# Kernel tuning notes

Measured on AMD Instinct MI355X. Metric: run time of the kernel, lower is better.

The kernel has to match this reference:

```python
import jax, jax.numpy as jnp
import numpy as np

N = 20000        # nodes
E = 320000       # edges (before self-loops)
V = 5000         # vocab size for each of the 5 categorical fields
L = 20           # padded token list length per node
SF = 16          # scalar feature count
ED = 32          # embedding_dim
HC = 128         # hidden_channels
NH = 4           # num_heads (conv1)
B = 8            # graphs in batch
DIN = SF + 5 * ED  # 176


def setup_inputs() -> dict:
    key = jax.random.key(0)
    ks = jax.random.split(key, 24)
    inp = {
        "x_scalar": jax.random.normal(ks[0], (N, SF), jnp.float32),
        "x_opcode": jax.random.randint(ks[1], (N, L), 0, V),
        "x_source": jax.random.randint(ks[2], (N, L), 0, V),
        "x_sink": jax.random.randint(ks[3], (N, L), 0, V),
        "x_string_manip": jax.random.randint(ks[4], (N, L), 0, V),
        "x_payload": jax.random.randint(ks[5], (N, L), 0, V),
        "edge_index": jax.random.randint(ks[6], (2, E), 0, N),
        "batch": jnp.sort(jax.random.randint(ks[7], (N,), 0, B)),
        # embedding tables (padding row 0 contributes nothing via the mask)
        "emb_opcode": jax.random.normal(ks[8], (V, ED), jnp.float32),
        "emb_source": jax.random.normal(ks[9], (V, ED), jnp.float32),
        "emb_sink": jax.random.normal(ks[10], (V, ED), jnp.float32),
        "emb_string_manip": jax.random.normal(ks[11], (V, ED), jnp.float32),
        "emb_payload": jax.random.normal(ks[12], (V, ED), jnp.float32),
        # LayerNorm params
        "ln_g": jnp.ones((DIN,), jnp.float32),
        "ln_b": jnp.zeros((DIN,), jnp.float32),
        # GATConv 1: in=DIN, out=HC, heads=NH
        "W1": jax.random.normal(ks[13], (DIN, NH * HC), jnp.float32) / np.sqrt(DIN),
        "a_src1": jax.random.normal(ks[14], (NH, HC), jnp.float32) / np.sqrt(HC),
        "a_dst1": jax.random.normal(ks[15], (NH, HC), jnp.float32) / np.sqrt(HC),
        "b1": jnp.zeros((NH * HC,), jnp.float32),
        # GATConv 2: in=NH*HC, out=HC, heads=1
        "W2": jax.random.normal(ks[16], (NH * HC, HC), jnp.float32) / np.sqrt(NH * HC),
        "a_src2": jax.random.normal(ks[17], (1, HC), jnp.float32) / np.sqrt(HC),
        "a_dst2": jax.random.normal(ks[18], (1, HC), jnp.float32) / np.sqrt(HC),
        "b2": jnp.zeros((HC,), jnp.float32),
    }
    return inp


def _masked_mean(table, idx):
    # embeds * (idx != 0) summed over token dim, divided by token count
    emb = table[idx]                                   # [N, L, ED]
    mask = (idx != 0).astype(table.dtype)[..., None]   # [N, L, 1]
    return (emb * mask).sum(1) / (mask.sum(1) + 1e-9)


def _layer_norm(x, g, b, eps=1e-5):
    mu = x.mean(-1, keepdims=True)
    var = ((x - mu) ** 2).mean(-1, keepdims=True)
    return (x - mu) * jax.lax.rsqrt(var + eps) * g + b


def _gat(x, src, dst, W, a_src, a_dst, bias, n):
    # PyG GATConv (eval mode: attention dropout off), self-loops already in src/dst
    h_, c = a_src.shape
    h = (x @ W).reshape(n, h_, c)                      # [N, H, C]
    al_s = (h * a_src).sum(-1)                         # [N, H]
    al_d = (h * a_dst).sum(-1)                         # [N, H]
    e = jax.nn.leaky_relu(al_s[src] + al_d[dst], 0.2)  # [E, H]
    m = jax.ops.segment_max(e, dst, num_segments=n)    # per-dst max for stability
    ex = jnp.exp(e - m[dst])
    den = jax.ops.segment_sum(ex, dst, num_segments=n)
    alpha = ex / (den[dst] + 1e-16)                    # per-dst softmax
    msg = h[src] * alpha[:, :, None]                   # [E, H, C]
    out = jax.ops.segment_sum(msg, dst, num_segments=n)
    return out.reshape(n, h_ * c) + bias


def reference(x_scalar, x_opcode, x_source, x_sink, x_string_manip, x_payload,
              edge_index, batch,
              emb_opcode, emb_source, emb_sink, emb_string_manip, emb_payload,
              ln_g, ln_b, W1, a_src1, a_dst1, b1, W2, a_src2, a_dst2, b2):
    n = x_scalar.shape[0]
    feats = jnp.concatenate([
        x_scalar,
        _masked_mean(emb_opcode, x_opcode),
        _masked_mean(emb_source, x_source),
        _masked_mean(emb_sink, x_sink),
        _masked_mean(emb_string_manip, x_string_manip),
        _masked_mean(emb_payload, x_payload),
    ], axis=1)                                         # [N, DIN]
    # GATConv adds self-loops by default
    loops = jnp.arange(n, dtype=edge_index.dtype)
    src = jnp.concatenate([edge_index[0], loops])
    dst = jnp.concatenate([edge_index[1], loops])
    x = jax.nn.elu(_gat(_layer_norm(feats, ln_g, ln_b), src, dst, W1, a_src1, a_dst1, b1, n))
    x = jax.nn.elu(_gat(x, src, dst, W2, a_src2, a_dst2, b2, n))
    return jax.ops.segment_max(x, batch, num_segments=B)  # global_max_pool -> [B, HC]
```

## Files before the change

kernel.cpp:

```cpp
#include <hip/hip_runtime.h>
#include <math.h>

#define SF 16
#define ED 32
#define LTOK 20
#define DIN 176
#define KP1 192
#define HC 128

typedef _Float16 f16x8 __attribute__((ext_vector_type(8)));
typedef float f32x4 __attribute__((ext_vector_type(4)));

static __device__ __forceinline__ float leaky02(float x) { return x >= 0.f ? x : 0.2f * x; }
static __device__ __forceinline__ float eluf(float x)    { return x > 0.f ? x : expm1f(x); }
static __device__ __forceinline__ unsigned short f2h(float f)
{
  _Float16 h = (_Float16)f;
  return __builtin_bit_cast(unsigned short, h);
}
static __device__ __forceinline__ float h2f(unsigned short u)
{
  return (float)__builtin_bit_cast(_Float16, u);
}
static __device__ __forceinline__ float readlane_f(float v, int j)
{
  return __int_as_float(__builtin_amdgcn_readlane(__float_as_int(v), j));
}

__global__ __launch_bounds__(256)
void prep_combined_kernel(const float* __restrict__ W1, const float* __restrict__ W2,
                          unsigned short* __restrict__ W1t, unsigned short* __restrict__ W2t,
                          const float* __restrict__ as1, const float* __restrict__ ad1,
                          float* __restrict__ vs, float* __restrict__ vd,
                          int* __restrict__ deg, unsigned* __restrict__ pool,
                          int N, int poolN)
{
  const int nb1 = (512 * KP1 + 255) / 256;
  const int nb2 = (HC * 512 + 255) / 256;
  const int nb3 = (N + 255) / 256;
  const int nb4 = (poolN + 255) / 256;
  int bid = blockIdx.x;
  if (bid < nb1) {
    int i = bid * 256 + threadIdx.x;
    if (i < 512 * KP1) {
      int n = i / KP1, k = i - n * KP1;
      W1t[i] = f2h((k < DIN) ? W1[(size_t)k * 512 + n] : 0.f);
    }
    return;
  }
  bid -= nb1;
  if (bid < nb2) {
    int i = bid * 256 + threadIdx.x;
    if (i < HC * 512) {
      int n = i / 512, k = i - n * 512;
      W2t[i] = f2h(W2[(size_t)k * HC + n]);
    }
    return;
  }
  bid -= nb2;
  if (bid < nb3) {
    int i = bid * 256 + threadIdx.x;
    if (i < N) deg[i] = 0;
    return;
  }
  bid -= nb3;
  if (bid < nb4) {
    int i = bid * 256 + threadIdx.x;
    if (i < poolN) pool[i] = 0x00800000u;
    return;
  }
  bid -= nb4;
  {
    int k = bid;
    int h = threadIdx.x >> 6, lane = threadIdx.x & 63;
    const float* row = W1 + (size_t)k * 512 + h * HC;
    float s = row[lane] * as1[h * HC + lane] + row[lane + 64] * as1[h * HC + lane + 64];
    float d = row[lane] * ad1[h * HC + lane] + row[lane + 64] * ad1[h * HC + lane + 64];
    #pragma unroll
    for (int off = 32; off; off >>= 1) { s += __shfl_down(s, off); d += __shfl_down(d, off); }
    if (lane == 0) { vs[k * 4 + h] = s; vd[k * 4 + h] = d; }
  }
}

__global__ __launch_bounds__(256)
void feat_ln_kernel(const float* __restrict__ xs,
                    const int* __restrict__ i0, const int* __restrict__ i1,
                    const int* __restrict__ i2, const int* __restrict__ i3,
                    const int* __restrict__ i4,
                    const float* __restrict__ e0, const float* __restrict__ e1,
                    const float* __restrict__ e2, const float* __restrict__ e3,
                    const float* __restrict__ e4,
                    const float* __restrict__ g, const float* __restrict__ b,
                    const float4* __restrict__ vs, const float4* __restrict__ vd,
                    unsigned short* __restrict__ out,
                    float* __restrict__ als, float* __restrict__ ald, int N)
{
  __shared__ int toks[4][5 * LTOK];
  int w = threadIdx.x >> 6, l = threadIdx.x & 63;
  int n = blockIdx.x * 4 + w;
  if (n >= N) return;

  for (int q = l; q < 5 * LTOK; q += 64) {
    int f = q / LTOK, j = q - f * LTOK;
    const int* ip = (f == 0) ? i0 : (f == 1) ? i1 : (f == 2) ? i2 : (f == 3) ? i3 : i4;
    toks[w][q] = ip[n * LTOK + j];
  }

  float v[3];
  #pragma unroll
  for (int r = 0; r < 3; ++r) {
    int c = l + r * 64;
    float val = 0.f;
    if (c < SF) {
      val = xs[n * SF + c];
    } else if (c < DIN) {
      int f  = (c - SF) >> 5;
      int ch = (c - SF) & 31;
      const float* ep = (f == 0) ? e0 : (f == 1) ? e1 : (f == 2) ? e2 : (f == 3) ? e3 : e4;
      float vals[LTOK];
      #pragma unroll
      for (int j = 0; j < LTOK; ++j)
        vals[j] = ep[toks[w][f * LTOK + j] * ED + ch];
      float sum = 0.f, cnt = 0.f;
      #pragma unroll
      for (int j = 0; j < LTOK; ++j)
        if (toks[w][f * LTOK + j] != 0) { sum += vals[j]; cnt += 1.f; }
      val = sum / (cnt + 1e-9f);
    }
    v[r] = val;
  }

  float p  = v[0] + v[1] + v[2];
  float p2 = v[0] * v[0] + v[1] * v[1] + v[2] * v[2];
  #pragma unroll
  for (int off = 32; off; off >>= 1) { p += __shfl_xor(p, off); p2 += __shfl_xor(p2, off); }
  float mu   = p * (1.f / DIN);
  float var  = fmaxf(p2 * (1.f / DIN) - mu * mu, 0.f);
  float rstd = rsqrtf(var + 1e-5f);

  float pr[8] = {0.f, 0.f, 0.f, 0.f, 0.f, 0.f, 0.f, 0.f};
  #pragma unroll
  for (int r = 0; r < 3; ++r) {
    int c = l + r * 64;
    float y = 0.f;
    if (c < DIN) {
      y = (v[r] - mu) * rstd * g[c] + b[c];
      float4 s4 = vs[c], d4 = vd[c];
      pr[0] += y * s4.x; pr[1] += y * s4.y; pr[2] += y * s4.z; pr[3] += y * s4.w;
      pr[4] += y * d4.x; pr[5] += y * d4.y; pr[6] += y * d4.z; pr[7] += y * d4.w;
    }
    if (c < KP1) out[(size_t)n * KP1 + c] = f2h(y);
  }
  #pragma unroll
  for (int j = 0; j < 8; ++j)
    #pragma unroll
    for (int off = 32; off; off >>= 1) pr[j] += __shfl_xor(pr[j], off);
  if (l == 0) {
    als[n * 4 + 0] = pr[0]; als[n * 4 + 1] = pr[1];
    als[n * 4 + 2] = pr[2]; als[n * 4 + 3] = pr[3];
    ald[n * 4 + 0] = pr[4]; ald[n * 4 + 1] = pr[5];
    ald[n * 4 + 2] = pr[6]; ald[n * 4 + 3] = pr[7];
  }
}

__global__ void count_kernel(const int* __restrict__ ei, int E, int N, int* __restrict__ deg)
{
  int e = blockIdx.x * blockDim.x + threadIdx.x;
  if (e < E + N) {
    int dst = (e < E) ? ei[E + e] : (e - E);
    atomicAdd(&deg[dst], 1);
  }
}

__global__ __launch_bounds__(1024)
void scan_kernel(const int* __restrict__ deg, int* __restrict__ rowptr,
                 int* __restrict__ fill, int N)
{
  __shared__ int sums[1024];
  int t = threadIdx.x;
  int CH = (N + 1023) >> 10;
  int base = t * CH;
  int s = 0;
  for (int i = 0; i < CH; ++i) if (base + i < N) s += deg[base + i];
  sums[t] = s;
  __syncthreads();
  for (int off = 1; off < 1024; off <<= 1) {
    int v = (t >= off) ? sums[t - off] : 0;
    __syncthreads();
    sums[t] += v;
    __syncthreads();
  }
  int run = sums[t] - s;
  for (int i = 0; i < CH; ++i) {
    if (base + i < N) {
      rowptr[base + i] = run;
      fill[base + i]   = run;
      run += deg[base + i];
    }
  }
  if (t == 1023) rowptr[N] = run;
}

__global__ void scatter_kernel(const int* __restrict__ ei, int E, int N,
                               int* __restrict__ fill, int* __restrict__ csr_src)
{
  int e = blockIdx.x * blockDim.x + threadIdx.x;
  if (e < E + N) {
    int src, dst;
    if (e < E) { src = ei[e]; dst = ei[E + e]; }
    else       { src = dst = e - E; }
    int pos = atomicAdd(&fill[dst], 1);
    csr_src[pos] = src;
  }
}

static __device__ __forceinline__ void agg_passB(
    const unsigned short* __restrict__ F, int cnt, int srcA, float4 wA,
    int half, int sub, float acc[4][8])
{
  for (int j = 0; j < cnt; j += 2) {
    int j1 = j + 1;
    bool has1 = j1 < cnt;
    int s0 = __builtin_amdgcn_readlane(srcA, j);
    int s1 = has1 ? __builtin_amdgcn_readlane(srcA, j1) : s0;
    float w[4];
    float w0x = readlane_f(wA.x, j), w0y = readlane_f(wA.y, j);
    float w0z = readlane_f(wA.z, j), w0w = readlane_f(wA.w, j);
    float w1x = 0.f, w1y = 0.f, w1z = 0.f, w1w = 0.f;
    if (has1) {
      w1x = readlane_f(wA.x, j1); w1y = readlane_f(wA.y, j1);
      w1z = readlane_f(wA.z, j1); w1w = readlane_f(wA.w, j1);
    }
    w[0] = half ? w1x : w0x;  w[1] = half ? w1y : w0y;
    w[2] = half ? w1z : w0z;  w[3] = half ? w1w : w0w;
    int src = half ? s1 : s0;
    if (sub < 24) {
      int4 vv = *(const int4*)(F + (size_t)src * KP1 + sub * 8);
      float f[8];
      f[0] = h2f((unsigned short)(vv.x & 0xffff)); f[1] = h2f((unsigned short)((unsigned)vv.x >> 16));
      f[2] = h2f((unsigned short)(vv.y & 0xffff)); f[3] = h2f((unsigned short)((unsigned)vv.y >> 16));
      f[4] = h2f((unsigned short)(vv.z & 0xffff)); f[5] = h2f((unsigned short)((unsigned)vv.z >> 16));
      f[6] = h2f((unsigned short)(vv.w & 0xffff)); f[7] = h2f((unsigned short)((unsigned)vv.w >> 16));
      #pragma unroll
      for (int h = 0; h < 4; ++h)
        #pragma unroll
        for (int c = 0; c < 8; ++c)
          acc[h][c] += w[h] * f[c];
    }
  }
}

__global__ __launch_bounds__(256)
void agg_feat_kernel(const unsigned short* __restrict__ F,
                     const float4* __restrict__ als, const float4* __restrict__ ald,
                     const int* __restrict__ rowptr, const int* __restrict__ csr_src,
                     unsigned short* __restrict__ G, int N)
{
  int wv = threadIdx.x >> 6, lane = threadIdx.x & 63;
  int n = blockIdx.x * 4 + wv;
  if (n >= N) return;
  int rs = __builtin_amdgcn_readfirstlane(rowptr[n]);
  int re = __builtin_amdgcn_readfirstlane(rowptr[n + 1]);
  int cnt = re - rs;
  float4 ad4 = ald[n];
  float aldv[4] = { ad4.x, ad4.y, ad4.z, ad4.w };
  int half = lane >> 5, sub = lane & 31;
  float acc[4][8] = {};

  if (cnt <= 64) {
    int srcA = 0;
    float e[4] = { -1e30f, -1e30f, -1e30f, -1e30f };
    if (lane < cnt) {
      srcA = csr_src[rs + lane];
      float4 a4 = als[srcA];
      e[0] = leaky02(a4.x + aldv[0]); e[1] = leaky02(a4.y + aldv[1]);
      e[2] = leaky02(a4.z + aldv[2]); e[3] = leaky02(a4.w + aldv[3]);
    }
    float m[4] = { e[0], e[1], e[2], e[3] };
    #pragma unroll
    for (int off = 32; off; off >>= 1)
      #pragma unroll
      for (int h = 0; h < 4; ++h) m[h] = fmaxf(m[h], __shfl_xor(m[h], off));
    float ex[4];
    #pragma unroll
    for (int h = 0; h < 4; ++h) ex[h] = (lane < cnt) ? __expf(e[h] - m[h]) : 0.f;
    float den[4] = { ex[0], ex[1], ex[2], ex[3] };
    #pragma unroll
    for (int off = 32; off; off >>= 1)
      #pragma unroll
      for (int h = 0; h < 4; ++h) den[h] += __shfl_xor(den[h], off);
    float4 wA;
    wA.x = ex[0] / (den[0] + 1e-16f); wA.y = ex[1] / (den[1] + 1e-16f);
    wA.z = ex[2] / (den[2] + 1e-16f); wA.w = ex[3] / (den[3] + 1e-16f);
    agg_passB(F, cnt, srcA, wA, half, sub, acc);
  } else {
    float m[4], s[4];
    #pragma unroll
    for (int h = 0; h < 4; ++h) { m[h] = -1e30f; s[h] = 0.f; }
    for (int i = rs + lane; i < re; i += 64) {
      int src = csr_src[i];
      float4 a4 = als[src];
      float av[4] = { a4.x, a4.y, a4.z, a4.w };
      #pragma unroll
      for (int h = 0; h < 4; ++h) {
        float e = leaky02(av[h] + aldv[h]);
        float Mx = fmaxf(m[h], e);
        s[h] = s[h] * __expf(m[h] - Mx) + __expf(e - Mx);
        m[h] = Mx;
      }
    }
    #pragma unroll
    for (int off = 32; off; off >>= 1) {
      #pragma unroll
      for (int h = 0; h < 4; ++h) {
        float m2 = __shfl_xor(m[h], off);
        float s2 = __shfl_xor(s[h], off);
        float Mx = fmaxf(m[h], m2);
        s[h] = s[h] * __expf(m[h] - Mx) + s2 * __expf(m2 - Mx);
        m[h] = Mx;
      }
    }
    float inv[4];
    #pragma unroll
    for (int h = 0; h < 4; ++h) inv[h] = 1.f / (s[h] + 1e-16f);
    for (int c0 = rs; c0 < re; c0 += 64) {
      int ccnt = min(64, re - c0);
      int srcA = 0;
      float4 wA = make_float4(0.f, 0.f, 0.f, 0.f);
      if (lane < ccnt) {
        srcA = csr_src[c0 + lane];
        float4 a4 = als[srcA];
        wA.x = __expf(leaky02(a4.x + aldv[0]) - m[0]) * inv[0];
        wA.y = __expf(leaky02(a4.y + aldv[1]) - m[1]) * inv[1];
        wA.z = __expf(leaky02(a4.z + aldv[2]) - m[2]) * inv[2];
        wA.w = __expf(leaky02(a4.w + aldv[3]) - m[3]) * inv[3];
      }
      agg_passB(F, ccnt, srcA, wA, half, sub, acc);
    }
  }

  #pragma unroll
  for (int h = 0; h < 4; ++h)
    #pragma unroll
    for (int c = 0; c < 8; ++c)
      acc[h][c] += __shfl_xor(acc[h][c], 32);
  if (lane < 24) {
    #pragma unroll
    for (int h = 0; h < 4; ++h) {
      int4 o;
      o.x = (int)f2h(acc[h][0]) | ((int)f2h(acc[h][1]) << 16);
      o.y = (int)f2h(acc[h][2]) | ((int)f2h(acc[h][3]) << 16);
      o.z = (int)f2h(acc[h][4]) | ((int)f2h(acc[h][5]) << 16);
      o.w = (int)f2h(acc[h][6]) | ((int)f2h(acc[h][7]) << 16);
      *(int4*)&G[((size_t)h * N + n) * KP1 + lane * 8] = o;
    }
  }
}

template<int KPad>
__global__ __launch_bounds__(256)
void gemm_f16_kernel(const unsigned short* __restrict__ A, const unsigned short* __restrict__ Bt,
                     unsigned short* __restrict__ C, int M, int Nc,
                     size_t aStrideZ, size_t bStrideZ, int cColStrideZ,
                     const float* __restrict__ bias, int act,
                     const float* __restrict__ la_s, const float* __restrict__ la_d,
                     float* __restrict__ lout_s, float* __restrict__ lout_d)
{
  A  += blockIdx.z * aStrideZ;
  Bt += blockIdx.z * bStrideZ;
  int colZ = blockIdx.z * cColStrideZ;

  __shared__ __align__(16) unsigned short As[4][128][8];
  __shared__ __align__(16) unsigned short Bs[4][128][8];
  __shared__ float ls[128][2];
  int tid  = threadIdx.x;
  int lane = tid & 63, wave = tid >> 6;
  int wm = (wave >> 1) << 6, wn = (wave & 1) << 6;
  int bm = blockIdx.y << 7, bn = blockIdx.x << 7;

  int srow = tid >> 1;
  int skc  = (tid & 1) << 1;
  const unsigned short* Arow = A  + (size_t)(bm + srow) * KPad + skc * 8;
  const unsigned short* Brow = Bt + (size_t)(bn + srow) * KPad + skc * 8;
  bool aok = (bm + srow) < M;

  f32x4 acc[4][4];
  #pragma unroll
  for (int m = 0; m < 4; ++m)
    #pragma unroll
    for (int n2 = 0; n2 < 4; ++n2) acc[m][n2] = (f32x4){0.f, 0.f, 0.f, 0.f};

  int kc  = lane >> 4;
  int r16 = lane & 15;

  for (int k0 = 0; k0 < KPad; k0 += 32) {
    int4 av0 = make_int4(0, 0, 0, 0), av1 = make_int4(0, 0, 0, 0);
    if (aok) {
      av0 = *(const int4*)(Arow + k0);
      av1 = *(const int4*)(Arow + k0 + 8);
    }
    int4 bv0 = *(const int4*)(Brow + k0);
    int4 bv1 = *(const int4*)(Brow + k0 + 8);
    __syncthreads();
    *(int4*)&As[skc][srow][0]     = av0;
    *(int4*)&As[skc + 1][srow][0] = av1;
    *(int4*)&Bs[skc][srow][0]     = bv0;
    *(int4*)&Bs[skc + 1][srow][0] = bv1;
    __syncthreads();

    f16x8 af[4], bfr[4];
    #pragma unroll
    for (int m = 0; m < 4; ++m)  af[m]  = *(const f16x8*)&As[kc][wm + m * 16 + r16][0];
    #pragma unroll
    for (int n2 = 0; n2 < 4; ++n2) bfr[n2] = *(const f16x8*)&Bs[kc][wn + n2 * 16 + r16][0];
    #pragma unroll
    for (int m = 0; m < 4; ++m)
      #pragma unroll
      for (int n2 = 0; n2 < 4; ++n2)
        acc[m][n2] = __builtin_amdgcn_mfma_f32_16x16x32_f16(af[m], bfr[n2], acc[m][n2], 0, 0, 0);
  }

  int rq = lane >> 4;
  #pragma unroll
  for (int m = 0; m < 4; ++m) {
    #pragma unroll
    for (int r = 0; r < 4; ++r) {
      int row = bm + wm + m * 16 + rq * 4 + r;
      if (row < M) {
        #pragma unroll
        for (int n2 = 0; n2 < 4; ++n2) {
          int col = colZ + bn + wn + n2 * 16 + r16;
          float val = acc[m][n2][r];
          if (bias) val += bias[col];
          if (act)  val = eluf(val);
          C[(size_t)row * Nc + col] = f2h(val);
        }
      }
    }
  }

  if (lout_s) {
    float ps[4][4] = {}, pd[4][4] = {};
    #pragma unroll
    for (int m = 0; m < 4; ++m)
      #pragma unroll
      for (int r = 0; r < 4; ++r)
        #pragma unroll
        for (int n2 = 0; n2 < 4; ++n2) {
          int col = wn + n2 * 16 + r16;
          float val = acc[m][n2][r];
          ps[m][r] += val * la_s[col];
          pd[m][r] += val * la_d[col];
        }
    #pragma unroll
    for (int off = 1; off < 16; off <<= 1)
      #pragma unroll
      for (int m = 0; m < 4; ++m)
        #pragma unroll
        for (int r = 0; r < 4; ++r) {
          ps[m][r] += __shfl_xor(ps[m][r], off);
          pd[m][r] += __shfl_xor(pd[m][r], off);
        }
    if (r16 == 0 && wn == 0) {
      #pragma unroll
      for (int m = 0; m < 4; ++m)
        #pragma unroll
        for (int r = 0; r < 4; ++r) {
          int rl = wm + m * 16 + rq * 4 + r;
          ls[rl][0] = ps[m][r];
          ls[rl][1] = pd[m][r];
        }
    }
    __syncthreads();
    if (r16 == 0 && wn != 0) {
      #pragma unroll
      for (int m = 0; m < 4; ++m)
        #pragma unroll
        for (int r = 0; r < 4; ++r) {
          int rl = wm + m * 16 + rq * 4 + r;
          int row = bm + rl;
          if (row < M) {
            lout_s[row] = ls[rl][0] + ps[m][r];
            lout_d[row] = ls[rl][1] + pd[m][r];
          }
        }
    }
  }
}

__global__ __launch_bounds__(256)
void agg_h2_kernel(const unsigned short* __restrict__ H,
                   const float* __restrict__ al_s, const float* __restrict__ al_d,
                   const int* __restrict__ rowptr, const int* __restrict__ csr_src,
                   const float* __restrict__ bias, unsigned short* __restrict__ out, int N)
{
  int wv = threadIdx.x >> 6, lane = threadIdx.x & 63;
  int n = blockIdx.x * 4 + wv;
  if (n >= N) return;
  int rs = __builtin_amdgcn_readfirstlane(rowptr[n]);
  int re = __builtin_amdgcn_readfirstlane(rowptr[n + 1]);
  int cnt = re - rs;
  float ald = al_d[n];
  int half = lane >> 5, sub = lane & 31;
  float acc[4] = {0.f, 0.f, 0.f, 0.f};

  auto passB = [&](int c2, int srcA, float wAl) {
    for (int j = 0; j < c2; j += 2) {
      int j1 = j + 1;
      bool has1 = j1 < c2;
      int s0 = __builtin_amdgcn_readlane(srcA, j);
      int s1 = has1 ? __builtin_amdgcn_readlane(srcA, j1) : s0;
      float w0 = readlane_f(wAl, j);
      float w1 = has1 ? readlane_f(wAl, j1) : 0.f;
      float wgt = half ? w1 : w0;
      int src = half ? s1 : s0;
      int2 vv = *(const int2*)(H + (size_t)src * HC + sub * 4);
      acc[0] += wgt * h2f((unsigned short)(vv.x & 0xffff));
      acc[1] += wgt * h2f((unsigned short)((unsigned)vv.x >> 16));
      acc[2] += wgt * h2f((unsigned short)(vv.y & 0xffff));
      acc[3] += wgt * h2f((unsigned short)((unsigned)vv.y >> 16));
    }
  };

  if (cnt <= 64) {
    int srcA = 0;
    float e = -1e30f;
    if (lane < cnt) {
      srcA = csr_src[rs + lane];
      e = leaky02(al_s[srcA] + ald);
    }
    float m = e;
    #pragma unroll
    for (int off = 32; off; off >>= 1) m = fmaxf(m, __shfl_xor(m, off));
    float ex = (lane < cnt) ? __expf(e - m) : 0.f;
    float den = ex;
    #pragma unroll
    for (int off = 32; off; off >>= 1) den += __shfl_xor(den, off);
    passB(cnt, srcA, ex / (den + 1e-16f));
  } else {
    float m = -1e30f, s = 0.f;
    for (int i = rs + lane; i < re; i += 64) {
      int src = csr_src[i];
      float e = leaky02(al_s[src] + ald);
      float Mx = fmaxf(m, e);
      s = s * __expf(m - Mx) + __expf(e - Mx);
      m = Mx;
    }
    #pragma unroll
    for (int off = 32; off; off >>= 1) {
      float m2 = __shfl_xor(m, off);
      float s2 = __shfl_xor(s, off);
      float Mx = fmaxf(m, m2);
      s = s * __expf(m - Mx) + s2 * __expf(m2 - Mx);
      m = Mx;
    }
    float inv_den = 1.f / (s + 1e-16f);
    for (int c0 = rs; c0 < re; c0 += 64) {
      int ccnt = min(64, re - c0);
      int srcA = 0;
      float wAl = 0.f;
      if (lane < ccnt) {
        srcA = csr_src[c0 + lane];
        wAl = __expf(leaky02(al_s[srcA] + ald) - m) * inv_den;
      }
      passB(ccnt, srcA, wAl);
    }
  }

  #pragma unroll
  for (int c = 0; c < 4; ++c) acc[c] += __shfl_xor(acc[c], 32);
  if (lane < 32) {
    float o0 = eluf(acc[0] + bias[sub * 4 + 0]);
    float o1 = eluf(acc[1] + bias[sub * 4 + 1]);
    float o2 = eluf(acc[2] + bias[sub * 4 + 2]);
    float o3 = eluf(acc[3] + bias[sub * 4 + 3]);
    int2 o;
    o.x = (int)f2h(o0) | ((int)f2h(o1) << 16);
    o.y = (int)f2h(o2) | ((int)f2h(o3) << 16);
    *(int2*)&out[(size_t)n * HC + sub * 4] = o;
  }
}

static __device__ __forceinline__ unsigned enc_f(float f)
{
  unsigned u = __float_as_uint(f);
  return (u & 0x80000000u) ? ~u : (u | 0x80000000u);
}
static __device__ __forceinline__ float dec_f(unsigned u)
{
  return (u & 0x80000000u) ? __uint_as_float(u & 0x7fffffffu) : __uint_as_float(~u);
}

#define PNPB 128
__global__ __launch_bounds__(256)
void pool_seg_kernel(const unsigned short* __restrict__ x, const int* __restrict__ batch,
                     unsigned* __restrict__ pool, int N)
{
  int cp = (threadIdx.x & 63) * 2;
  int g  = threadIdx.x >> 6;
  int n0 = blockIdx.x * PNPB;
  int n1 = min(n0 + PNPB, N);
  int curb = -1;
  float m0 = 0.f, m1 = 0.f;
  for (int n = n0 + g; n < n1; n += 4) {
    int bg = batch[n];
    ushort2 v = *(const ushort2*)&x[(size_t)n * HC + cp];
    float v0 = h2f(v.x), v1 = h2f(v.y);
    if (bg != curb) {
      if (curb >= 0) {
        atomicMax(&pool[curb * HC + cp],     enc_f(m0));
        atomicMax(&pool[curb * HC + cp + 1], enc_f(m1));
      }
      curb = bg; m0 = v0; m1 = v1;
    } else {
      m0 = fmaxf(m0, v0);
      m1 = fmaxf(m1, v1);
    }
  }
  if (curb >= 0) {
    atomicMax(&pool[curb * HC + cp],     enc_f(m0));
    atomicMax(&pool[curb * HC + cp + 1], enc_f(m1));
  }
}

__global__ void pool_final_kernel(const unsigned* __restrict__ pool, float* __restrict__ out, int n)
{
  int i = blockIdx.x * blockDim.x + threadIdx.x;
  if (i < n) out[i] = dec_f(pool[i]);
}

extern "C" void kernel_launch(void* const* d_in, const int* in_sizes, int n_in,
                              void* d_out, int out_size, void* d_ws, size_t ws_size,
                              hipStream_t stream)
{
  const float* x_scalar = (const float*)d_in[0];
  const int* i0 = (const int*)d_in[1];
  const int* i1 = (const int*)d_in[2];
  const int* i2 = (const int*)d_in[3];
  const int* i3 = (const int*)d_in[4];
  const int* i4 = (const int*)d_in[5];
  const int* ei = (const int*)d_in[6];
  const int* batch = (const int*)d_in[7];
  const float* e0 = (const float*)d_in[8];
  const float* e1 = (const float*)d_in[9];
  const float* e2 = (const float*)d_in[10];
  const float* e3 = (const float*)d_in[11];
  const float* e4 = (const float*)d_in[12];
  const float* ln_g = (const float*)d_in[13];
  const float* ln_b = (const float*)d_in[14];
  const float* W1 = (const float*)d_in[15];
  const float* as1 = (const float*)d_in[16];
  const float* ad1 = (const float*)d_in[17];
  const float* b1 = (const float*)d_in[18];
  const float* W2 = (const float*)d_in[19];
  const float* as2 = (const float*)d_in[20];
  const float* ad2 = (const float*)d_in[21];
  const float* b2 = (const float*)d_in[22];

  const int N  = in_sizes[0] / SF;
  const int E  = in_sizes[6] / 2;
  const int Et = E + N;
  const int Bg = out_size / HC;
  const int MT = (N + 127) / 128;

  char* w = (char*)d_ws;
  auto alloc = [&](size_t bytes) -> char* {
    char* p = w;
    w += (bytes + 255) & ~(size_t)255;
    return p;
  };
  unsigned short* featsb = (unsigned short*)alloc((size_t)N * KP1 * 2);
  unsigned short* G      = (unsigned short*)alloc((size_t)4 * N * KP1 * 2);
  unsigned short* X2b    = (unsigned short*)alloc((size_t)N * 512 * 2);
  unsigned short* H2b    = (unsigned short*)alloc((size_t)N * HC * 2);
  unsigned short* X3b    = (unsigned short*)alloc((size_t)N * HC * 2);
  unsigned short* W1t    = (unsigned short*)alloc((size_t)512 * KP1 * 2);
  unsigned short* W2t    = (unsigned short*)alloc((size_t)HC * 512 * 2);
  float* vs      = (float*)alloc((size_t)KP1 * 4 * 4);
  float* vd      = (float*)alloc((size_t)KP1 * 4 * 4);
  float* als1    = (float*)alloc((size_t)N * 4 * 4);
  float* ald1    = (float*)alloc((size_t)N * 4 * 4);
  float* als2    = (float*)alloc((size_t)N * 4);
  float* ald2    = (float*)alloc((size_t)N * 4);
  int*   deg     = (int*)alloc((size_t)N * 4);
  int*   rowptr  = (int*)alloc((size_t)(N + 1) * 4);
  int*   fill    = (int*)alloc((size_t)N * 4);
  int*   csr_src = (int*)alloc((size_t)Et * 4);
  unsigned* pool = (unsigned*)alloc((size_t)Bg * HC * 4);

  {
    int nb1 = (512 * KP1 + 255) / 256;
    int nb2 = (HC * 512 + 255) / 256;
    int nb3 = (N + 255) / 256;
    int nb4 = (Bg * HC + 255) / 256;
    prep_combined_kernel<<<nb1 + nb2 + nb3 + nb4 + DIN, 256, 0, stream>>>(
        W1, W2, W1t, W2t, as1, ad1, vs, vd, deg, pool, N, Bg * HC);
  }

  feat_ln_kernel<<<(N + 3) / 4, 256, 0, stream>>>(x_scalar, i0, i1, i2, i3, i4,
                                                  e0, e1, e2, e3, e4, ln_g, ln_b,
                                                  (const float4*)vs, (const float4*)vd,
                                                  featsb, als1, ald1, N);

  count_kernel<<<(Et + 255) / 256, 256, 0, stream>>>(ei, E, N, deg);
  scan_kernel<<<1, 1024, 0, stream>>>(deg, rowptr, fill, N);
  scatter_kernel<<<(Et + 255) / 256, 256, 0, stream>>>(ei, E, N, fill, csr_src);

  agg_feat_kernel<<<(N + 3) / 4, 256, 0, stream>>>(featsb, (const float4*)als1,
                                                   (const float4*)ald1,
                                                   rowptr, csr_src, G, N);
  gemm_f16_kernel<KP1><<<dim3(1, MT, 4), 256, 0, stream>>>(
      G, W1t, X2b, N, 512, (size_t)N * KP1, (size_t)HC * KP1, HC, b1, 1,
      nullptr, nullptr, nullptr, nullptr);

  gemm_f16_kernel<512><<<dim3(1, MT, 1), 256, 0, stream>>>(
      X2b, W2t, H2b, N, HC, 0, 0, 0, nullptr, 0,
      as2, ad2, als2, ald2);
  agg_h2_kernel<<<(N + 3) / 4, 256, 0, stream>>>(H2b, als2, ald2, rowptr, csr_src, b2, X3b, N);

  pool_seg_kernel<<<(N + PNPB - 1) / PNPB, 256, 0, stream>>>(X3b, batch, pool, N);
  pool_final_kernel<<<(Bg * HC + 255) / 256, 256, 0, stream>>>(pool, (float*)d_out, Bg * HC);
}
```

Before: 258.9 us.

## Use packed fp16 dot2 with paired-edge weights in GAT aggregation kernels

Both GAT aggregation kernels stop splitting the wave into two halves that each handle alternate edges. Every lane now owns a contiguous feature slice across all edges, and the two edges of each pair are interleaved with byte permutes. The attention weights for an edge pair are packed into fp16x2 and applied with v_dot2 (fdot2), which halves the FMA count, and the final cross-half shuffle reduction is removed. The cost is lower weight precision (fp16 softmax weights), twice as many narrower loads per lane, and 16 idle lanes in layer 1.

```diff
diff --git a/kernel.cpp b/kernel.cpp
--- a/kernel.cpp
+++ b/kernel.cpp
@@ -9,7 +9,14 @@
 #define HC 128
 
 typedef _Float16 f16x8 __attribute__((ext_vector_type(8)));
+typedef _Float16 f16x2 __attribute__((ext_vector_type(2)));
 typedef float f32x4 __attribute__((ext_vector_type(4)));
+
+#if defined(__has_builtin)
+#if __has_builtin(__builtin_amdgcn_fdot2)
+#define HAVE_FDOT2 1
+#endif
+#endif
 
 static __device__ __forceinline__ float leaky02(float x) { return x >= 0.f ? x : 0.2f * x; }
 static __device__ __forceinline__ float eluf(float x)    { return x > 0.f ? x : expm1f(x); }
@@ -26,6 +33,17 @@
 {
   return __int_as_float(__builtin_amdgcn_readlane(__float_as_int(v), j));
 }
+static __device__ __forceinline__ unsigned readlane_u(unsigned v, int j)
+{
+  return (unsigned)__builtin_amdgcn_readlane((int)v, j);
+}
+#ifdef HAVE_FDOT2
+static __device__ __forceinline__ float dot2(unsigned w, unsigned f, float c)
+{
+  return __builtin_amdgcn_fdot2(__builtin_bit_cast(f16x2, w),
+                                __builtin_bit_cast(f16x2, f), c, false);
+}
+#endif
 
 __global__ __launch_bounds__(256)
 void prep_combined_kernel(const float* __restrict__ W1, const float* __restrict__ W2,
@@ -214,42 +232,6 @@
   }
 }
 
-static __device__ __forceinline__ void agg_passB(
-    const unsigned short* __restrict__ F, int cnt, int srcA, float4 wA,
-    int half, int sub, float acc[4][8])
-{
-  for (int j = 0; j < cnt; j += 2) {
-    int j1 = j + 1;
-    bool has1 = j1 < cnt;
-    int s0 = __builtin_amdgcn_readlane(srcA, j);
-    int s1 = has1 ? __builtin_amdgcn_readlane(srcA, j1) : s0;
-    float w[4];
-    float w0x = readlane_f(wA.x, j), w0y = readlane_f(wA.y, j);
-    float w0z = readlane_f(wA.z, j), w0w = readlane_f(wA.w, j);
-    float w1x = 0.f, w1y = 0.f, w1z = 0.f, w1w = 0.f;
-    if (has1) {
-      w1x = readlane_f(wA.x, j1); w1y = readlane_f(wA.y, j1);
-      w1z = readlane_f(wA.z, j1); w1w = readlane_f(wA.w, j1);
-    }
-    w[0] = half ? w1x : w0x;  w[1] = half ? w1y : w0y;
-    w[2] = half ? w1z : w0z;  w[3] = half ? w1w : w0w;
-    int src = half ? s1 : s0;
-    if (sub < 24) {
-      int4 vv = *(const int4*)(F + (size_t)src * KP1 + sub * 8);
-      float f[8];
-      f[0] = h2f((unsigned short)(vv.x & 0xffff)); f[1] = h2f((unsigned short)((unsigned)vv.x >> 16));
-      f[2] = h2f((unsigned short)(vv.y & 0xffff)); f[3] = h2f((unsigned short)((unsigned)vv.y >> 16));
-      f[4] = h2f((unsigned short)(vv.z & 0xffff)); f[5] = h2f((unsigned short)((unsigned)vv.z >> 16));
-      f[6] = h2f((unsigned short)(vv.w & 0xffff)); f[7] = h2f((unsigned short)((unsigned)vv.w >> 16));
-      #pragma unroll
-      for (int h = 0; h < 4; ++h)
-        #pragma unroll
-        for (int c = 0; c < 8; ++c)
-          acc[h][c] += w[h] * f[c];
-    }
-  }
-}
-
 __global__ __launch_bounds__(256)
 void agg_feat_kernel(const unsigned short* __restrict__ F,
                      const float4* __restrict__ als, const float4* __restrict__ ald,
@@ -264,8 +246,58 @@
   int cnt = re - rs;
   float4 ad4 = ald[n];
   float aldv[4] = { ad4.x, ad4.y, ad4.z, ad4.w };
-  int half = lane >> 5, sub = lane & 31;
-  float acc[4][8] = {};
+
+  float acc[4][4] = {};
+  bool act = lane < 48;
+  const unsigned short* Fb = F + lane * 4;
+
+#ifdef HAVE_FDOT2
+  auto passB = [&](int srcA, unsigned pkw[4], int ccnt) {
+    for (int j = 0; j < ccnt; j += 2) {
+      int s0 = __builtin_amdgcn_readlane(srcA, j);
+      int s1 = __builtin_amdgcn_readlane(srcA, j + 1 < 64 ? j + 1 : j);
+      unsigned w0 = readlane_u(pkw[0], j);
+      unsigned w1 = readlane_u(pkw[1], j);
+      unsigned w2 = readlane_u(pkw[2], j);
+      unsigned w3 = readlane_u(pkw[3], j);
+      if (act) {
+        int2 a0 = *(const int2*)(Fb + (size_t)s0 * KP1);
+        int2 a1 = *(const int2*)(Fb + (size_t)s1 * KP1);
+        unsigned pA = __builtin_amdgcn_perm((unsigned)a0.x, (unsigned)a1.x, 0x01000504u);
+        unsigned pB = __builtin_amdgcn_perm((unsigned)a0.x, (unsigned)a1.x, 0x03020706u);
+        unsigned pC = __builtin_amdgcn_perm((unsigned)a0.y, (unsigned)a1.y, 0x01000504u);
+        unsigned pD = __builtin_amdgcn_perm((unsigned)a0.y, (unsigned)a1.y, 0x03020706u);
+        acc[0][0] = dot2(w0, pA, acc[0][0]); acc[0][1] = dot2(w0, pB, acc[0][1]);
+        acc[0][2] = dot2(w0, pC, acc[0][2]); acc[0][3] = dot2(w0, pD, acc[0][3]);
+        acc[1][0] = dot2(w1, pA, acc[1][0]); acc[1][1] = dot2(w1, pB, acc[1][1]);
+        acc[1][2] = dot2(w1, pC, acc[1][2]); acc[1][3] = dot2(w1, pD, acc[1][3]);
+        acc[2][0] = dot2(w2, pA, acc[2][0]); acc[2][1] = dot2(w2, pB, acc[2][1]);
+        acc[2][2] = dot2(w2, pC, acc[2][2]); acc[2][3] = dot2(w2, pD, acc[2][3]);
+        acc[3][0] = dot2(w3, pA, acc[3][0]); acc[3][1] = dot2(w3, pB, acc[3][1]);
+        acc[3][2] = dot2(w3, pC, acc[3][2]); acc[3][3] = dot2(w3, pD, acc[3][3]);
+      }
+    }
+  };
+#else
+  auto passB = [&](int srcA, float wf[4], int ccnt) {
+    for (int j = 0; j < ccnt; ++j) {
+      int src = __builtin_amdgcn_readlane(srcA, j);
+      float q0 = readlane_f(wf[0], j), q1 = readlane_f(wf[1], j);
+      float q2 = readlane_f(wf[2], j), q3 = readlane_f(wf[3], j);
+      if (act) {
+        int2 a0 = *(const int2*)(Fb + (size_t)src * KP1);
+        float f0 = h2f((unsigned short)(a0.x & 0xffff));
+        float f1 = h2f((unsigned short)((unsigned)a0.x >> 16));
+        float f2v = h2f((unsigned short)(a0.y & 0xffff));
+        float f3 = h2f((unsigned short)((unsigned)a0.y >> 16));
+        acc[0][0] += q0 * f0; acc[0][1] += q0 * f1; acc[0][2] += q0 * f2v; acc[0][3] += q0 * f3;
+        acc[1][0] += q1 * f0; acc[1][1] += q1 * f1; acc[1][2] += q1 * f2v; acc[1][3] += q1 * f3;
+        acc[2][0] += q2 * f0; acc[2][1] += q2 * f1; acc[2][2] += q2 * f2v; acc[2][3] += q2 * f3;
+        acc[3][0] += q3 * f0; acc[3][1] += q3 * f1; acc[3][2] += q3 * f2v; acc[3][3] += q3 * f3;
+      }
+    }
+  };
+#endif
 
   if (cnt <= 64) {
     int srcA = 0;
@@ -281,18 +313,29 @@
     for (int off = 32; off; off >>= 1)
       #pragma unroll
       for (int h = 0; h < 4; ++h) m[h] = fmaxf(m[h], __shfl_xor(m[h], off));
-    float ex[4];
-    #pragma unroll
-    for (int h = 0; h < 4; ++h) ex[h] = (lane < cnt) ? __expf(e[h] - m[h]) : 0.f;
-    float den[4] = { ex[0], ex[1], ex[2], ex[3] };
+    float w[4];
+    #pragma unroll
+    for (int h = 0; h < 4; ++h) w[h] = (lane < cnt) ? __expf(e[h] - m[h]) : 0.f;
+    float den[4] = { w[0], w[1], w[2], w[3] };
     #pragma unroll
     for (int off = 32; off; off >>= 1)
       #pragma unroll
       for (int h = 0; h < 4; ++h) den[h] += __shfl_xor(den[h], off);
-    float4 wA;
-    wA.x = ex[0] / (den[0] + 1e-16f); wA.y = ex[1] / (den[1] + 1e-16f);
-    wA.z = ex[2] / (den[2] + 1e-16f); wA.w = ex[3] / (den[3] + 1e-16f);
-    agg_passB(F, cnt, srcA, wA, half, sub, acc);
+    #pragma unroll
+    for (int h = 0; h < 4; ++h) w[h] /= (den[h] + 1e-16f);
+#ifdef HAVE_FDOT2
+    unsigned pkw[4];
+    #pragma unroll
+    for (int h = 0; h < 4; ++h) {
+      float wn = __shfl_xor(w[h], 1);
+      float we = (lane & 1) ? wn : w[h];
+      float wo = (lane & 1) ? w[h] : wn;
+      pkw[h] = (unsigned)f2h(we) | ((unsigned)f2h(wo) << 16);
+    }
+    passB(srcA, pkw, cnt);
+#else
+    passB(srcA, w, cnt);
+#endif
   } else {
     float m[4], s[4];
     #pragma unroll
@@ -323,36 +366,41 @@
     float inv[4];
     #pragma unroll
     for (int h = 0; h < 4; ++h) inv[h] = 1.f / (s[h] + 1e-16f);
-    for (int c0 = rs; c0 < re; c0 += 64) {
-      int ccnt = min(64, re - c0);
+    for (int b0 = rs; b0 < re; b0 += 64) {
+      int bcnt = min(64, re - b0);
       int srcA = 0;
-      float4 wA = make_float4(0.f, 0.f, 0.f, 0.f);
-      if (lane < ccnt) {
-        srcA = csr_src[c0 + lane];
+      float w[4] = {0.f, 0.f, 0.f, 0.f};
+      if (lane < bcnt) {
+        srcA = csr_src[b0 + lane];
         float4 a4 = als[srcA];
-        wA.x = __expf(leaky02(a4.x + aldv[0]) - m[0]) * inv[0];
-        wA.y = __expf(leaky02(a4.y + aldv[1]) - m[1]) * inv[1];
-        wA.z = __expf(leaky02(a4.z + aldv[2]) - m[2]) * inv[2];
-        wA.w = __expf(leaky02(a4.w + aldv[3]) - m[3]) * inv[3];
-      }
-      agg_passB(F, ccnt, srcA, wA, half, sub, acc);
-    }
-  }
-
-  #pragma unroll
-  for (int h = 0; h < 4; ++h)
-    #pragma unroll
-    for (int c = 0; c < 8; ++c)
-      acc[h][c] += __shfl_xor(acc[h][c], 32);
-  if (lane < 24) {
+        w[0] = __expf(leaky02(a4.x + aldv[0]) - m[0]) * inv[0];
+        w[1] = __expf(leaky02(a4.y + aldv[1]) - m[1]) * inv[1];
+        w[2] = __expf(leaky02(a4.z + aldv[2]) - m[2]) * inv[2];
+        w[3] = __expf(leaky02(a4.w + aldv[3]) - m[3]) * inv[3];
+      }
+#ifdef HAVE_FDOT2
+      unsigned pkw[4];
+      #pragma unroll
+      for (int h = 0; h < 4; ++h) {
+        float wn = __shfl_xor(w[h], 1);
+        float we = (lane & 1) ? wn : w[h];
+        float wo = (lane & 1) ? w[h] : wn;
+        pkw[h] = (unsigned)f2h(we) | ((unsigned)f2h(wo) << 16);
+      }
+      passB(srcA, pkw, bcnt);
+#else
+      passB(srcA, w, bcnt);
+#endif
+    }
+  }
+
+  if (act) {
     #pragma unroll
     for (int h = 0; h < 4; ++h) {
-      int4 o;
+      int2 o;
       o.x = (int)f2h(acc[h][0]) | ((int)f2h(acc[h][1]) << 16);
       o.y = (int)f2h(acc[h][2]) | ((int)f2h(acc[h][3]) << 16);
-      o.z = (int)f2h(acc[h][4]) | ((int)f2h(acc[h][5]) << 16);
-      o.w = (int)f2h(acc[h][6]) | ((int)f2h(acc[h][7]) << 16);
-      *(int4*)&G[((size_t)h * N + n) * KP1 + lane * 8] = o;
+      *(int2*)&G[((size_t)h * N + n) * KP1 + lane * 4] = o;
     }
   }
 }
@@ -501,26 +549,34 @@
   int re = __builtin_amdgcn_readfirstlane(rowptr[n + 1]);
   int cnt = re - rs;
   float ald = al_d[n];
-  int half = lane >> 5, sub = lane & 31;
-  float acc[4] = {0.f, 0.f, 0.f, 0.f};
-
-  auto passB = [&](int c2, int srcA, float wAl) {
-    for (int j = 0; j < c2; j += 2) {
-      int j1 = j + 1;
-      bool has1 = j1 < c2;
+  float acc0 = 0.f, acc1 = 0.f;
+  const unsigned short* Hb = H + lane * 2;
+
+#ifdef HAVE_FDOT2
+  auto passB = [&](int srcA, unsigned pkw, int ccnt) {
+    for (int j = 0; j < ccnt; j += 2) {
       int s0 = __builtin_amdgcn_readlane(srcA, j);
-      int s1 = has1 ? __builtin_amdgcn_readlane(srcA, j1) : s0;
-      float w0 = readlane_f(wAl, j);
-      float w1 = has1 ? readlane_f(wAl, j1) : 0.f;
-      float wgt = half ? w1 : w0;
-      int src = half ? s1 : s0;
-      int2 vv = *(const int2*)(H + (size_t)src * HC + sub * 4);
-      acc[0] += wgt * h2f((unsigned short)(vv.x & 0xffff));
-      acc[1] += wgt * h2f((unsigned short)((unsigned)vv.x >> 16));
-      acc[2] += wgt * h2f((unsigned short)(vv.y & 0xffff));
-      acc[3] += wgt * h2f((unsigned short)((unsigned)vv.y >> 16));
+      int s1 = __builtin_amdgcn_readlane(srcA, j + 1 < 64 ? j + 1 : j);
+      unsigned pw = readlane_u(pkw, j);
+      unsigned a0 = *(const unsigned*)(Hb + (size_t)s0 * HC);
+      unsigned a1 = *(const unsigned*)(Hb + (size_t)s1 * HC);
+      unsigned p0 = __builtin_amdgcn_perm(a0, a1, 0x01000504u);
+      unsigned p1 = __builtin_amdgcn_perm(a0, a1, 0x03020706u);
+      acc0 = dot2(pw, p0, acc0);
+      acc1 = dot2(pw, p1, acc1);
     }
   };
+#else
+  auto passB = [&](int srcA, float wf, int ccnt) {
+    for (int j = 0; j < ccnt; ++j) {
+      int src = __builtin_amdgcn_readlane(srcA, j);
+      float wgt = readlane_f(wf, j);
+      unsigned a0 = *(const unsigned*)(Hb + (size_t)src * HC);
+      acc0 += wgt * h2f((unsigned short)(a0 & 0xffff));
+      acc1 += wgt * h2f((unsigned short)(a0 >> 16));
+    }
+  };
+#endif
 
   if (cnt <= 64) {
     int srcA = 0;
@@ -532,11 +588,20 @@
     float m = e;
     #pragma unroll
     for (int off = 32; off; off >>= 1) m = fmaxf(m, __shfl_xor(m, off));
-    float ex = (lane < cnt) ? __expf(e - m) : 0.f;
-    float den = ex;
+    float w = (lane < cnt) ? __expf(e - m) : 0.f;
+    float den = w;
     #pragma unroll
     for (int off = 32; off; off >>= 1) den += __shfl_xor(den, off);
-    passB(cnt, srcA, ex / (den + 1e-16f));
+    w /= (den + 1e-16f);
+#ifdef HAVE_FDOT2
+    float wn2 = __shfl_xor(w, 1);
+    float we = (lane & 1) ? wn2 : w;
+    float wo = (lane & 1) ? w : wn2;
+    unsigned pkw = (unsigned)f2h(we) | ((unsigned)f2h(wo) << 16);
+    passB(srcA, pkw, cnt);
+#else
+    passB(srcA, w, cnt);
+#endif
   } else {
     float m = -1e30f, s = 0.f;
     for (int i = rs + lane; i < re; i += 64) {
@@ -558,27 +623,27 @@
     for (int c0 = rs; c0 < re; c0 += 64) {
       int ccnt = min(64, re - c0);
       int srcA = 0;
-      float wAl = 0.f;
+      float w = 0.f;
       if (lane < ccnt) {
         srcA = csr_src[c0 + lane];
-        wAl = __expf(leaky02(al_s[srcA] + ald) - m) * inv_den;
-      }
-      passB(ccnt, srcA, wAl);
-    }
-  }
-
-  #pragma unroll
-  for (int c = 0; c < 4; ++c) acc[c] += __shfl_xor(acc[c], 32);
-  if (lane < 32) {
-    float o0 = eluf(acc[0] + bias[sub * 4 + 0]);
-    float o1 = eluf(acc[1] + bias[sub * 4 + 1]);
-    float o2 = eluf(acc[2] + bias[sub * 4 + 2]);
-    float o3 = eluf(acc[3] + bias[sub * 4 + 3]);
-    int2 o;
-    o.x = (int)f2h(o0) | ((int)f2h(o1) << 16);
-    o.y = (int)f2h(o2) | ((int)f2h(o3) << 16);
-    *(int2*)&out[(size_t)n * HC + sub * 4] = o;
-  }
+        w = __expf(leaky02(al_s[srcA] + ald) - m) * inv_den;
+      }
+#ifdef HAVE_FDOT2
+      float wn2 = __shfl_xor(w, 1);
+      float we = (lane & 1) ? wn2 : w;
+      float wo = (lane & 1) ? w : wn2;
+      unsigned pkw = (unsigned)f2h(we) | ((unsigned)f2h(wo) << 16);
+      passB(srcA, pkw, ccnt);
+#else
+      passB(srcA, w, ccnt);
+#endif
+    }
+  }
+
+  float o0 = eluf(acc0 + bias[lane * 2 + 0]);
+  float o1 = eluf(acc1 + bias[lane * 2 + 1]);
+  unsigned o = (unsigned)f2h(o0) | ((unsigned)f2h(o1) << 16);
+  *(unsigned*)&out[(size_t)n * HC + lane * 2] = o;
 }
 
 static __device__ __forceinline__ unsigned enc_f(float f)
```

New measurement: 244.9 us. 5.4% less time.
